# Optimization experiments

Measured on AMD Instinct MI355X. Metric: run time of the kernel, lower is better.

Reference implementation:

```python
import jax, jax.numpy as jnp
import numpy as np

INDIM, HID, OUTDIM, T = 28, 128, 10, 28

def setup_inputs() -> dict:
    key = jax.random.key(0)
    ks = jax.random.split(key, 7)
    B = 65536
    bound1 = 1.0 / np.sqrt(INDIM)
    bound2 = 1.0 / np.sqrt(2 * HID)
    bound3 = 1.0 / np.sqrt(HID)
    return {
        "x": jax.random.normal(ks[0], (B, 784), dtype=jnp.float32),
        "W1": jax.random.uniform(ks[1], (INDIM, HID), jnp.float32, -bound1, bound1),
        "b1": jax.random.uniform(ks[2], (HID,), jnp.float32, -bound1, bound1),
        "W2": jax.random.uniform(ks[3], (2 * HID, HID), jnp.float32, -bound2, bound2),
        "b2": jax.random.uniform(ks[4], (HID,), jnp.float32, -bound2, bound2),
        "W3": jax.random.uniform(ks[5], (HID, OUTDIM), jnp.float32, -bound3, bound3),
        "b3": jax.random.uniform(ks[6], (OUTDIM,), jnp.float32, -bound3, bound3),
    }

def reference(x, W1, b1, W2, b2, W3, b3):
    B = x.shape[0]
    # (B, 784) -> (T, B, 28): scan over the 28 rows of each image
    rows = jnp.transpose(x.reshape(B, T, INDIM), (1, 0, 2))
    # W2 split: first HID rows multiply linear1 output, last HID rows multiply hidden state
    W2a, W2b = W2[:HID], W2[HID:]

    def step(h, row):
        t = row @ W1 + b1                      # (B, HID)
        h_new = jax.nn.relu(t @ W2a + h @ W2b + b2)  # concat(t, h) @ W2 == t@W2a + h@W2b
        return h_new, None

    h0 = jnp.zeros((B, HID), dtype=x.dtype)
    h_final, _ = jax.lax.scan(step, h0, rows)
    return h_final @ W3 + b3
```

## Files before the change

kernel.cpp:

```cpp
#include <hip/hip_runtime.h>

#define BTOT 65536
#define TST  28
#define PACK_DW 180
#define WXL_OFF (64 * PACK_DW)

typedef __attribute__((ext_vector_type(8))) short bf16x8;
typedef __attribute__((ext_vector_type(4))) float f32x4;
typedef __attribute__((ext_vector_type(2))) unsigned int u32x2;

__device__ __forceinline__ unsigned int f2bf(float f) {
    unsigned u = __float_as_uint(f);
    u += 0x7fff + ((u >> 16) & 1);
    return u >> 16;
}
__device__ __forceinline__ unsigned int pk2bf(float a, float b) {
    return f2bf(a) | (f2bf(b) << 16);
}
__device__ __forceinline__ bf16x8 cvt8(f32x4 a, f32x4 b) {
    union { unsigned int u[4]; bf16x8 v; } r;
    asm("v_cvt_pk_bf16_f32 %0, %1, %2" : "=v"(r.u[0]) : "v"(a[0]), "v"(a[1]));
    asm("v_cvt_pk_bf16_f32 %0, %1, %2" : "=v"(r.u[1]) : "v"(a[2]), "v"(a[3]));
    asm("v_cvt_pk_bf16_f32 %0, %1, %2" : "=v"(r.u[2]) : "v"(b[0]), "v"(b[1]));
    asm("v_cvt_pk_bf16_f32 %0, %1, %2" : "=v"(r.u[3]) : "v"(b[2]), "v"(b[3]));
    return r.v;
}

__global__ void pack1(const float* __restrict__ W1, const float* __restrict__ b1,
                      const float* __restrict__ W2, const float* __restrict__ b2,
                      const float* __restrict__ W3, const float* __restrict__ b3,
                      unsigned int* __restrict__ ws) {
    float* WxL = (float*)(ws + WXL_OFF);
    const int bid = blockIdx.x, tid = threadIdx.x;
    if (bid < 29) {
        const int k = bid, n = tid;
        float s = 0.f;
        if (k < 28) {
            for (int m = 0; m < 128; ++m) s += W1[k * 128 + m] * W2[m * 128 + n];
        } else {
            s = b2[n];
            for (int m = 0; m < 128; ++m) s += b1[m] * W2[m * 128 + n];
        }
        WxL[k * 128 + n] = s;
        if (k == 28) { WxL[29*128+n] = 0.f; WxL[30*128+n] = 0.f; WxL[31*128+n] = 0.f; }
    } else if (bid == 29) {
        if (tid < 64) {
            const int lr = tid & 15, kh = tid >> 4;
            unsigned int* P = ws + tid * PACK_DW;
            for (int kk = 0; kk < 4; ++kk)
                for (int t8 = 0; t8 < 8; ++t8)
                    for (int jd = 0; jd < 4; ++jd) {
                        const int k = 128 + kk * 32 + kh * 8 + jd * 2;
                        const int n = t8 * 16 + lr;
                        P[(kk * 8 + t8) * 4 + jd] =
                            pk2bf(W2[k * 128 + n], W2[(k + 1) * 128 + n]);
                    }
        }
    } else {
        if (tid < 64) {
            const int lr = tid & 15, kh = tid >> 4;
            unsigned int* P = ws + tid * PACK_DW;
            for (int kk = 0; kk < 4; ++kk)
                for (int jd = 0; jd < 4; ++jd) {
                    const int k = kk * 32 + kh * 8 + jd * 2;
                    float lo = (lr < 10) ? W3[k * 10 + lr] : 0.f;
                    float hi = (lr < 10) ? W3[(k + 1) * 10 + lr] : 0.f;
                    P[160 + kk * 4 + jd] = pk2bf(lo, hi);
                }
            for (int j = 0; j < 4; ++j) {
                const int o = kh * 4 + j;
                P[176 + j] = __float_as_uint((o < 10) ? b3[o] : 0.f);
            }
        }
    }
}

__global__ void pack2(unsigned int* __restrict__ ws) {
    const int tid = threadIdx.x;
    if (tid < 64) {
        const float* WxL = (const float*)(ws + WXL_OFF);
        const int lr = tid & 15, kh = tid >> 4;
        unsigned int* P = ws + tid * PACK_DW;
        for (int t8 = 0; t8 < 8; ++t8)
            for (int jd = 0; jd < 4; ++jd) {
                const int k = kh * 8 + jd * 2, n = t8 * 16 + lr;
                P[128 + t8 * 4 + jd] = pk2bf(WxL[k * 128 + n], WxL[(k + 1) * 128 + n]);
            }
    }
}

__global__ __launch_bounds__(64, 2) void rnn_kernel(
    const float* __restrict__ x, const unsigned int* __restrict__ wsPack,
    float* __restrict__ out)
{
    __shared__ __align__(16) unsigned int Hs[1024];
    const int lane = threadIdx.x;
    const int lr = lane & 15, kh = lane >> 4;
    const int r0 = blockIdx.x * 16;

    const unsigned int* P = wsPack + lane * PACK_DW;
    bf16x8 w2b[4][8], wx[8];
    #pragma unroll
    for (int kk = 0; kk < 4; ++kk)
        #pragma unroll
        for (int t8 = 0; t8 < 8; ++t8)
            w2b[kk][t8] = *(const bf16x8*)(P + (kk * 8 + t8) * 4);
    #pragma unroll
    for (int t8 = 0; t8 < 8; ++t8) wx[t8] = *(const bf16x8*)(P + 128 + t8 * 4);

    unsigned wAddr[8];
    #pragma unroll
    for (int t8 = 0; t8 < 8; ++t8)
        wAddr[t8] = (t8 >> 1) * 256 + (2 * (t8 & 1) + (kh >> 1)) * 64
                  + lr * 4 + (kh & 1) * 2;

    const f32x4 onec = {1.f, 0.f, 0.f, 0.f};
    const float* xr = x + (size_t)(r0 + lr) * 784 + 8 * kh;
    f32x4 xa = *(const f32x4*)xr;
    f32x4 xc = (kh < 3) ? *(const f32x4*)(xr + 4) : onec;
    bf16x8 xb = cvt8(xa, xc);
    const f32x4 z4 = {0.f, 0.f, 0.f, 0.f};

    f32x4 acc[8];
    bf16x8 hbv[4];
    f32x4 na, nc;

#define ST(T8) do {                                                         \
        f32x4 v = acc[T8];                                                  \
        v[0] = fmaxf(v[0], 0.f); v[1] = fmaxf(v[1], 0.f);                   \
        v[2] = fmaxf(v[2], 0.f); v[3] = fmaxf(v[3], 0.f);                   \
        unsigned lo, hi;                                                    \
        asm("v_cvt_pk_bf16_f32 %0, %1, %2" : "=v"(lo) : "v"(v[0]), "v"(v[1])); \
        asm("v_cvt_pk_bf16_f32 %0, %1, %2" : "=v"(hi) : "v"(v[2]), "v"(v[3])); \
        u32x2 st = {lo, hi};                                                \
        *(u32x2*)&Hs[wAddr[T8]] = st;                                       \
    } while (0)
#define RD(KK) hbv[KK] = *(const bf16x8*)&Hs[(KK) * 256 + lane * 4]
#define STRD  ST(0); ST(1); RD(0); ST(2); ST(3); RD(1); \
              ST(4); ST(5); RD(2); ST(6); ST(7); RD(3)

    {
        const float* xp = xr + 28;
        na = *(const f32x4*)xp;
        nc = (kh < 3) ? *(const f32x4*)(xp + 4) : onec;
        __builtin_amdgcn_s_setprio(1);
        #pragma unroll
        for (int t8 = 0; t8 < 8; ++t8)
            acc[t8] = __builtin_amdgcn_mfma_f32_16x16x32_bf16(wx[t8], xb, z4, 0, 0, 0);
        __builtin_amdgcn_s_setprio(0);
        xb = cvt8(na, nc);
        STRD;
    }

    #pragma unroll 3
    for (int t = 1; t < TST; ++t) {
        const bool pf = (t + 1 < TST);
        if (pf) {
            const float* xp = xr + (t + 1) * 28;
            na = *(const f32x4*)xp;
            nc = (kh < 3) ? *(const f32x4*)(xp + 4) : onec;
        }
        __builtin_amdgcn_s_setprio(1);
        #pragma unroll
        for (int t8 = 0; t8 < 8; ++t8)
            acc[t8] = __builtin_amdgcn_mfma_f32_16x16x32_bf16(wx[t8], xb, z4, 0, 0, 0);
        #pragma unroll
        for (int kk = 0; kk < 4; ++kk)
            #pragma unroll
            for (int t8 = 0; t8 < 8; ++t8)
                acc[t8] = __builtin_amdgcn_mfma_f32_16x16x32_bf16(w2b[kk][t8], hbv[kk], acc[t8], 0, 0, 0);
        __builtin_amdgcn_s_setprio(0);
        if (pf) xb = cvt8(na, nc);
        STRD;
    }

    bf16x8 w3f[4];
    #pragma unroll
    for (int kk = 0; kk < 4; ++kk) w3f[kk] = *(const bf16x8*)(P + 160 + kk * 4);
    const float* bp = (const float*)(P + 176);
    f32x4 accO = {bp[0], bp[1], bp[2], bp[3]};
    #pragma unroll
    for (int kk = 0; kk < 4; ++kk)
        accO = __builtin_amdgcn_mfma_f32_16x16x32_bf16(w3f[kk], hbv[kk], accO, 0, 0, 0);
    float* op = out + (size_t)(r0 + lr) * 10 + kh * 4;
    #pragma unroll
    for (int j = 0; j < 4; ++j)
        if (kh * 4 + j < 10) op[j] = accO[j];

#undef ST
#undef RD
#undef STRD
}

extern "C" void kernel_launch(void* const* d_in, const int* in_sizes, int n_in,
                              void* d_out, int out_size, void* d_ws, size_t ws_size,
                              hipStream_t stream) {
    const float* x  = (const float*)d_in[0];
    const float* W1 = (const float*)d_in[1];
    const float* b1 = (const float*)d_in[2];
    const float* W2 = (const float*)d_in[3];
    const float* b2 = (const float*)d_in[4];
    const float* W3 = (const float*)d_in[5];
    const float* b3 = (const float*)d_in[6];
    unsigned int* ws = (unsigned int*)d_ws;

    pack1<<<31, 128, 0, stream>>>(W1, b1, W2, b2, W3, b3, ws);
    pack2<<<1, 64, 0, stream>>>(ws);
    rnn_kernel<<<BTOT / 16, 64, 0, stream>>>(x, ws, (float*)d_out);
}
```

Before: 77.66 us.

## Process two 16-row batch tiles per wave with interleaved MFMA chains

Each wavefront now handles 32 batch rows as two independent 16-row tiles, interleaving their MFMA chains so one tile's dependent accumulations hide the other's latency. The register-resident W2b and Wx fragments are reused across both tiles, and the grid is halved. Launch bounds drop to one wave per EU, which frees registers for the doubled accumulators and hidden-state fragments but lowers occupancy. The s_setprio hints are removed.

```diff
diff --git a/kernel.cpp b/kernel.cpp
--- a/kernel.cpp
+++ b/kernel.cpp
@@ -89,14 +89,16 @@
     }
 }
 
-__global__ __launch_bounds__(64, 2) void rnn_kernel(
+#define MFMA(a, b, c) __builtin_amdgcn_mfma_f32_16x16x32_bf16(a, b, c, 0, 0, 0)
+
+__global__ __launch_bounds__(64, 1) void rnn_kernel(
     const float* __restrict__ x, const unsigned int* __restrict__ wsPack,
     float* __restrict__ out)
 {
-    __shared__ __align__(16) unsigned int Hs[1024];
+    __shared__ __align__(16) unsigned int Hs[2][1024];
     const int lane = threadIdx.x;
     const int lr = lane & 15, kh = lane >> 4;
-    const int r0 = blockIdx.x * 16;
+    const int r0 = blockIdx.x * 32;
 
     const unsigned int* P = wsPack + lane * PACK_DW;
     bf16x8 w2b[4][8], wx[8];
@@ -115,63 +117,83 @@
                   + lr * 4 + (kh & 1) * 2;
 
     const f32x4 onec = {1.f, 0.f, 0.f, 0.f};
-    const float* xr = x + (size_t)(r0 + lr) * 784 + 8 * kh;
-    f32x4 xa = *(const f32x4*)xr;
-    f32x4 xc = (kh < 3) ? *(const f32x4*)(xr + 4) : onec;
-    bf16x8 xb = cvt8(xa, xc);
+    const float* xrA = x + (size_t)(r0 + lr) * 784 + 8 * kh;
+    const float* xrB = xrA + 16 * 784;
+    f32x4 qa = *(const f32x4*)xrA;
+    f32x4 qc = (kh < 3) ? *(const f32x4*)(xrA + 4) : onec;
+    bf16x8 xbA = cvt8(qa, qc);
+    qa = *(const f32x4*)xrB;
+    qc = (kh < 3) ? *(const f32x4*)(xrB + 4) : onec;
+    bf16x8 xbB = cvt8(qa, qc);
     const f32x4 z4 = {0.f, 0.f, 0.f, 0.f};
 
-    f32x4 acc[8];
-    bf16x8 hbv[4];
-    f32x4 na, nc;
-
-#define ST(T8) do {                                                         \
-        f32x4 v = acc[T8];                                                  \
+    f32x4 accA[8], accB[8];
+    bf16x8 hbvA[4], hbvB[4];
+    f32x4 naA, ncA, naB, ncB;
+    unsigned int* HsA = &Hs[0][0];
+    unsigned int* HsB = &Hs[1][0];
+
+#define ST1(HSP, ACC, T8) do {                                              \
+        f32x4 v = ACC[T8];                                                  \
         v[0] = fmaxf(v[0], 0.f); v[1] = fmaxf(v[1], 0.f);                   \
         v[2] = fmaxf(v[2], 0.f); v[3] = fmaxf(v[3], 0.f);                   \
         unsigned lo, hi;                                                    \
         asm("v_cvt_pk_bf16_f32 %0, %1, %2" : "=v"(lo) : "v"(v[0]), "v"(v[1])); \
         asm("v_cvt_pk_bf16_f32 %0, %1, %2" : "=v"(hi) : "v"(v[2]), "v"(v[3])); \
         u32x2 st = {lo, hi};                                                \
-        *(u32x2*)&Hs[wAddr[T8]] = st;                                       \
+        *(u32x2*)&(HSP)[wAddr[T8]] = st;                                    \
     } while (0)
-#define RD(KK) hbv[KK] = *(const bf16x8*)&Hs[(KK) * 256 + lane * 4]
-#define STRD  ST(0); ST(1); RD(0); ST(2); ST(3); RD(1); \
-              ST(4); ST(5); RD(2); ST(6); ST(7); RD(3)
+#define RD1(HSP, HBV, KK) HBV[KK] = *(const bf16x8*)&(HSP)[(KK) * 256 + lane * 4]
+#define STRD(HSP, ACC, HBV)                       \
+    ST1(HSP, ACC, 0); ST1(HSP, ACC, 1); RD1(HSP, HBV, 0); \
+    ST1(HSP, ACC, 2); ST1(HSP, ACC, 3); RD1(HSP, HBV, 1); \
+    ST1(HSP, ACC, 4); ST1(HSP, ACC, 5); RD1(HSP, HBV, 2); \
+    ST1(HSP, ACC, 6); ST1(HSP, ACC, 7); RD1(HSP, HBV, 3)
 
     {
-        const float* xp = xr + 28;
-        na = *(const f32x4*)xp;
-        nc = (kh < 3) ? *(const f32x4*)(xp + 4) : onec;
-        __builtin_amdgcn_s_setprio(1);
-        #pragma unroll
-        for (int t8 = 0; t8 < 8; ++t8)
-            acc[t8] = __builtin_amdgcn_mfma_f32_16x16x32_bf16(wx[t8], xb, z4, 0, 0, 0);
-        __builtin_amdgcn_s_setprio(0);
-        xb = cvt8(na, nc);
-        STRD;
-    }
-
-    #pragma unroll 3
+        const float* xp = xrA + 28;
+        naA = *(const f32x4*)xp;
+        ncA = (kh < 3) ? *(const f32x4*)(xp + 4) : onec;
+        xp = xrB + 28;
+        naB = *(const f32x4*)xp;
+        ncB = (kh < 3) ? *(const f32x4*)(xp + 4) : onec;
+        #pragma unroll
+        for (int t8 = 0; t8 < 8; ++t8) {
+            accA[t8] = MFMA(wx[t8], xbA, z4);
+            accB[t8] = MFMA(wx[t8], xbB, z4);
+        }
+        STRD(HsA, accA, hbvA);
+        STRD(HsB, accB, hbvB);
+        xbA = cvt8(naA, ncA);
+        xbB = cvt8(naB, ncB);
+    }
+
+    #pragma unroll 2
     for (int t = 1; t < TST; ++t) {
         const bool pf = (t + 1 < TST);
         if (pf) {
-            const float* xp = xr + (t + 1) * 28;
-            na = *(const f32x4*)xp;
-            nc = (kh < 3) ? *(const f32x4*)(xp + 4) : onec;
-        }
-        __builtin_amdgcn_s_setprio(1);
-        #pragma unroll
-        for (int t8 = 0; t8 < 8; ++t8)
-            acc[t8] = __builtin_amdgcn_mfma_f32_16x16x32_bf16(wx[t8], xb, z4, 0, 0, 0);
+            const float* xp = xrA + (t + 1) * 28;
+            naA = *(const f32x4*)xp;
+            ncA = (kh < 3) ? *(const f32x4*)(xp + 4) : onec;
+            xp = xrB + (t + 1) * 28;
+            naB = *(const f32x4*)xp;
+            ncB = (kh < 3) ? *(const f32x4*)(xp + 4) : onec;
+        }
+        #pragma unroll
+        for (int t8 = 0; t8 < 8; ++t8) {
+            accA[t8] = MFMA(wx[t8], xbA, z4);
+            accB[t8] = MFMA(wx[t8], xbB, z4);
+        }
         #pragma unroll
         for (int kk = 0; kk < 4; ++kk)
             #pragma unroll
-            for (int t8 = 0; t8 < 8; ++t8)
-                acc[t8] = __builtin_amdgcn_mfma_f32_16x16x32_bf16(w2b[kk][t8], hbv[kk], acc[t8], 0, 0, 0);
-        __builtin_amdgcn_s_setprio(0);
-        if (pf) xb = cvt8(na, nc);
-        STRD;
+            for (int t8 = 0; t8 < 8; ++t8) {
+                accA[t8] = MFMA(w2b[kk][t8], hbvA[kk], accA[t8]);
+                accB[t8] = MFMA(w2b[kk][t8], hbvB[kk], accB[t8]);
+            }
+        STRD(HsA, accA, hbvA);
+        STRD(HsB, accB, hbvB);
+        if (pf) { xbA = cvt8(naA, ncA); xbB = cvt8(naB, ncB); }
     }
 
     bf16x8 w3f[4];
@@ -181,14 +203,23 @@
     f32x4 accO = {bp[0], bp[1], bp[2], bp[3]};
     #pragma unroll
     for (int kk = 0; kk < 4; ++kk)
-        accO = __builtin_amdgcn_mfma_f32_16x16x32_bf16(w3f[kk], hbv[kk], accO, 0, 0, 0);
+        accO = MFMA(w3f[kk], hbvA[kk], accO);
     float* op = out + (size_t)(r0 + lr) * 10 + kh * 4;
     #pragma unroll
     for (int j = 0; j < 4; ++j)
         if (kh * 4 + j < 10) op[j] = accO[j];
 
-#undef ST
-#undef RD
+    accO = (f32x4){bp[0], bp[1], bp[2], bp[3]};
+    #pragma unroll
+    for (int kk = 0; kk < 4; ++kk)
+        accO = MFMA(w3f[kk], hbvB[kk], accO);
+    op = out + (size_t)(r0 + 16 + lr) * 10 + kh * 4;
+    #pragma unroll
+    for (int j = 0; j < 4; ++j)
+        if (kh * 4 + j < 10) op[j] = accO[j];
+
+#undef ST1
+#undef RD1
 #undef STRD
 }
 
@@ -206,5 +237,5 @@
 
     pack1<<<31, 128, 0, stream>>>(W1, b1, W2, b2, W3, b3, ws);
     pack2<<<1, 64, 0, stream>>>(ws);
-    rnn_kernel<<<BTOT / 16, 64, 0, stream>>>(x, ws, (float*)d_out);
-}
+    rnn_kernel<<<BTOT / 32, 64, 0, stream>>>(x, ws, (float*)d_out);
+}
```

Result: slower. 103.8 us (+33.7%).

## Keep RNN hidden state in registers by permuting W2b/W3 K ordering

Applied to the files above, without the earlier changes.

Removes the per-step LDS round trip for the hidden state. The MFMA output fragment is converted to bf16 and fed directly as the B operand of the next step's MFMAs. To make the accumulator layout match the operand layout, the packing of the recurrent weights and W3 along K is permuted to the order the output fragments naturally produce. This eliminates LDS writes and reads plus their latency on the serial recurrence critical path. Loop unroll also drops from 3 to 2.

```diff
diff --git a/kernel.cpp b/kernel.cpp
--- a/kernel.cpp
+++ b/kernel.cpp
@@ -7,7 +7,6 @@
 
 typedef __attribute__((ext_vector_type(8))) short bf16x8;
 typedef __attribute__((ext_vector_type(4))) float f32x4;
-typedef __attribute__((ext_vector_type(2))) unsigned int u32x2;
 
 __device__ __forceinline__ unsigned int f2bf(float f) {
     unsigned u = __float_as_uint(f);
@@ -25,6 +24,7 @@
     asm("v_cvt_pk_bf16_f32 %0, %1, %2" : "=v"(r.u[3]) : "v"(b[2]), "v"(b[3]));
     return r.v;
 }
+
 
 __global__ void pack1(const float* __restrict__ W1, const float* __restrict__ b1,
                       const float* __restrict__ W2, const float* __restrict__ b2,
@@ -50,10 +50,10 @@
             for (int kk = 0; kk < 4; ++kk)
                 for (int t8 = 0; t8 < 8; ++t8)
                     for (int jd = 0; jd < 4; ++jd) {
-                        const int k = 128 + kk * 32 + kh * 8 + jd * 2;
+                        const int s = kk * 32 + (jd >> 1) * 16 + kh * 4 + (jd & 1) * 2;
                         const int n = t8 * 16 + lr;
                         P[(kk * 8 + t8) * 4 + jd] =
-                            pk2bf(W2[k * 128 + n], W2[(k + 1) * 128 + n]);
+                            pk2bf(W2[(128 + s) * 128 + n], W2[(129 + s) * 128 + n]);
                     }
         }
     } else {
@@ -62,9 +62,9 @@
             unsigned int* P = ws + tid * PACK_DW;
             for (int kk = 0; kk < 4; ++kk)
                 for (int jd = 0; jd < 4; ++jd) {
-                    const int k = kk * 32 + kh * 8 + jd * 2;
-                    float lo = (lr < 10) ? W3[k * 10 + lr] : 0.f;
-                    float hi = (lr < 10) ? W3[(k + 1) * 10 + lr] : 0.f;
+                    const int s = kk * 32 + (jd >> 1) * 16 + kh * 4 + (jd & 1) * 2;
+                    float lo = (lr < 10) ? W3[s * 10 + lr] : 0.f;
+                    float hi = (lr < 10) ? W3[(s + 1) * 10 + lr] : 0.f;
                     P[160 + kk * 4 + jd] = pk2bf(lo, hi);
                 }
             for (int j = 0; j < 4; ++j) {
@@ -93,7 +93,6 @@
     const float* __restrict__ x, const unsigned int* __restrict__ wsPack,
     float* __restrict__ out)
 {
-    __shared__ __align__(16) unsigned int Hs[1024];
     const int lane = threadIdx.x;
     const int lr = lane & 15, kh = lane >> 4;
     const int r0 = blockIdx.x * 16;
@@ -107,12 +106,6 @@
             w2b[kk][t8] = *(const bf16x8*)(P + (kk * 8 + t8) * 4);
     #pragma unroll
     for (int t8 = 0; t8 < 8; ++t8) wx[t8] = *(const bf16x8*)(P + 128 + t8 * 4);
-
-    unsigned wAddr[8];
-    #pragma unroll
-    for (int t8 = 0; t8 < 8; ++t8)
-        wAddr[t8] = (t8 >> 1) * 256 + (2 * (t8 & 1) + (kh >> 1)) * 64
-                  + lr * 4 + (kh & 1) * 2;
 
     const f32x4 onec = {1.f, 0.f, 0.f, 0.f};
     const float* xr = x + (size_t)(r0 + lr) * 784 + 8 * kh;
@@ -122,22 +115,20 @@
     const f32x4 z4 = {0.f, 0.f, 0.f, 0.f};
 
     f32x4 acc[8];
-    bf16x8 hbv[4];
+    union HF { unsigned int u[4]; bf16x8 v; } hb[4];
     f32x4 na, nc;
 
-#define ST(T8) do {                                                         \
+#define CVT(T8) do {                                                        \
         f32x4 v = acc[T8];                                                  \
         v[0] = fmaxf(v[0], 0.f); v[1] = fmaxf(v[1], 0.f);                   \
         v[2] = fmaxf(v[2], 0.f); v[3] = fmaxf(v[3], 0.f);                   \
         unsigned lo, hi;                                                    \
         asm("v_cvt_pk_bf16_f32 %0, %1, %2" : "=v"(lo) : "v"(v[0]), "v"(v[1])); \
         asm("v_cvt_pk_bf16_f32 %0, %1, %2" : "=v"(hi) : "v"(v[2]), "v"(v[3])); \
-        u32x2 st = {lo, hi};                                                \
-        *(u32x2*)&Hs[wAddr[T8]] = st;                                       \
+        hb[(T8) >> 1].u[((T8) & 1) * 2]     = lo;                           \
+        hb[(T8) >> 1].u[((T8) & 1) * 2 + 1] = hi;                           \
     } while (0)
-#define RD(KK) hbv[KK] = *(const bf16x8*)&Hs[(KK) * 256 + lane * 4]
-#define STRD  ST(0); ST(1); RD(0); ST(2); ST(3); RD(1); \
-              ST(4); ST(5); RD(2); ST(6); ST(7); RD(3)
+#define CVTALL  CVT(0); CVT(1); CVT(2); CVT(3); CVT(4); CVT(5); CVT(6); CVT(7)
 
     {
         const float* xp = xr + 28;
@@ -149,10 +140,10 @@
             acc[t8] = __builtin_amdgcn_mfma_f32_16x16x32_bf16(wx[t8], xb, z4, 0, 0, 0);
         __builtin_amdgcn_s_setprio(0);
         xb = cvt8(na, nc);
-        STRD;
-    }
-
-    #pragma unroll 3
+        CVTALL;
+    }
+
+    #pragma unroll 2
     for (int t = 1; t < TST; ++t) {
         const bool pf = (t + 1 < TST);
         if (pf) {
@@ -168,10 +159,10 @@
         for (int kk = 0; kk < 4; ++kk)
             #pragma unroll
             for (int t8 = 0; t8 < 8; ++t8)
-                acc[t8] = __builtin_amdgcn_mfma_f32_16x16x32_bf16(w2b[kk][t8], hbv[kk], acc[t8], 0, 0, 0);
+                acc[t8] = __builtin_amdgcn_mfma_f32_16x16x32_bf16(w2b[kk][t8], hb[kk].v, acc[t8], 0, 0, 0);
         __builtin_amdgcn_s_setprio(0);
         if (pf) xb = cvt8(na, nc);
-        STRD;
+        CVTALL;
     }
 
     bf16x8 w3f[4];
@@ -181,15 +172,14 @@
     f32x4 accO = {bp[0], bp[1], bp[2], bp[3]};
     #pragma unroll
     for (int kk = 0; kk < 4; ++kk)
-        accO = __builtin_amdgcn_mfma_f32_16x16x32_bf16(w3f[kk], hbv[kk], accO, 0, 0, 0);
+        accO = __builtin_amdgcn_mfma_f32_16x16x32_bf16(w3f[kk], hb[kk].v, accO, 0, 0, 0);
     float* op = out + (size_t)(r0 + lr) * 10 + kh * 4;
     #pragma unroll
     for (int j = 0; j < 4; ++j)
         if (kh * 4 + j < 10) op[j] = accO[j];
 
-#undef ST
-#undef RD
-#undef STRD
+#undef CVT
+#undef CVTALL
 }
 
 extern "C" void kernel_launch(void* const* d_in, const int* in_sizes, int n_in,
```

Measured after the change: 71.75 us, median of 2. 7.6% less time.
